# Performance work log

Hardware: AMD Instinct MI355X
Metric: run time of the kernel (lower is better)

Reference implementation:

```python
import jax, jax.numpy as jnp
import numpy as np
import math

B, R, Q, K, C = 1, 128, 256, 256, 256
H, D = 8, 32  # no_heads, c_hidden; H*D == C


def setup_inputs() -> dict:
    key = jax.random.key(0)
    ks = jax.random.split(key, 11)
    s = 0.02
    return {
        "q_x": jax.random.normal(ks[0], (B, R, Q, C), jnp.float32),
        "k_x": jax.random.normal(ks[1], (B, R, K, C), jnp.float32),
        "v_x": jax.random.normal(ks[2], (B, R, K, C), jnp.float32),
        "bias": jax.random.normal(ks[3], (1, 1, H, Q, K), jnp.float32),
        # weights stored [in, out] (equivalent to torch Linear weight.T)
        "Wq": jax.random.normal(ks[4], (C, H * D), jnp.float32) * s,
        "Wk": jax.random.normal(ks[5], (C, H * D), jnp.float32) * s,
        "Wv": jax.random.normal(ks[6], (C, H * D), jnp.float32) * s,
        "Wo": jax.random.normal(ks[7], (H * D, C), jnp.float32) * s,
        "bo": jax.random.normal(ks[8], (C,), jnp.float32) * s,
        "Wg": jax.random.normal(ks[9], (C, H * D), jnp.float32) * s,
        "bg": jnp.ones((H * D,), jnp.float32),  # gating init: bias = 1
    }


def reference(q_x, k_x, v_x, bias, Wq, Wk, Wv, Wo, bo, Wg, bg):
    norm = 1.0 / math.sqrt(D)
    # projections -> [*, S, H, D]
    q = (q_x @ Wq).reshape(*q_x.shape[:-1], H, D)
    k = (k_x @ Wk).reshape(*k_x.shape[:-1], H, D)
    v = (v_x @ Wv).reshape(*v_x.shape[:-1], H, D)
    # scaled logits [*, H, Q, K] plus external bias
    a = jnp.einsum("...qhd,...khd->...hqk", q, k) * norm + bias
    a = jax.nn.softmax(a, axis=-1)
    # [*, Q, H, D]
    o = jnp.einsum("...hqk,...khd->...qhd", a, v)
    # sigmoid gate from query data
    g = jax.nn.sigmoid(q_x @ Wg + bg).reshape(o.shape)
    o = o * g
    o = o.reshape(*o.shape[:-2], H * D)
    return o @ Wo + bo
```

## Files before the change

### kernel.cpp

```cpp
#include <hip/hip_runtime.h>
#include <hip/hip_bf16.h>
#include <cstdint>
#include <cstddef>

typedef __attribute__((ext_vector_type(8))) short short8;
typedef __attribute__((ext_vector_type(4))) short s16x4;
typedef __attribute__((ext_vector_type(4))) unsigned short u16x4;
typedef __attribute__((ext_vector_type(8))) unsigned short u16x8;
typedef __attribute__((ext_vector_type(4))) float f32x4;
typedef __attribute__((ext_vector_type(4))) unsigned int u32x4;

__device__ __forceinline__ short bfbits(float f) {
    __bf16 h = (__bf16)f;
    return __builtin_bit_cast(short, h);
}
__device__ __forceinline__ float bf2f(unsigned short b) {
    union { uint32_t u; float f; } v; v.u = ((uint32_t)b) << 16;
    return v.f;
}
__device__ __forceinline__ unsigned int pack2(float x, float y) {
    return (unsigned int)(unsigned short)bfbits(x) |
           ((unsigned int)(unsigned short)bfbits(y) << 16);
}

__global__ __launch_bounds__(256) void prep_kernel(
    const float* __restrict__ Wq, const float* __restrict__ Wk,
    const float* __restrict__ Wv, const float* __restrict__ Wg,
    const float* __restrict__ Wo, unsigned short* __restrict__ wt,
    const float* __restrict__ bias, float* __restrict__ bt)
{
    int bid = blockIdx.x;
    int tid = threadIdx.x;
    if (bid < 80) {
        int mat  = bid >> 4;
        int tile = bid & 15;
        int k0 = (tile >> 2) * 64, n0 = (tile & 3) * 64;
        const float* W = (mat==0)?Wq:(mat==1)?Wk:(mat==2)?Wv:(mat==3)?Wg:Wo;
        __shared__ unsigned short T[64][72];
        int tx = tid & 15, ty = tid >> 4;
        #pragma unroll
        for (int j = 0; j < 4; ++j) {
            int kr = ty + j*16;
            f32x4 v = *(const f32x4*)(W + (size_t)(k0+kr)*256 + n0 + tx*4);
            #pragma unroll
            for (int e = 0; e < 4; ++e) T[tx*4+e][kr] = (unsigned short)bfbits(v[e]);
        }
        __syncthreads();
        #pragma unroll
        for (int j = 0; j < 4; ++j) {
            int nr = ty + j*16;
            int kk = k0 + tx*4;
            int dstk = kk;
            if (mat == 4) {
                int a = (kk >> 2) & 7;
                int hb = kk & ~31;
                dstk = hb + ((a < 4) ? 8*a : 8*(a-4) + 4);
            }
            u16x4 st;
            #pragma unroll
            for (int e = 0; e < 4; ++e) st[e] = T[nr][tx*4+e];
            *(u16x4*)(wt + ((size_t)mat*256 + n0+nr)*256 + dstk) = st;
        }
    } else {
        int hb = bid - 80;
        int h = hb >> 4, qt = hb & 15;
        int cc = tid >> 4, n = tid & 15;
        const float* src = bias + ((size_t)(h*256 + qt*16 + cc))*256 + n*16;
        float* dst = bt + ((size_t)(hb*16 + n))*256 + cc*16;
        #pragma unroll
        for (int q = 0; q < 4; ++q)
            *(f32x4*)(dst + q*4) = *(const f32x4*)(src + q*4);
    }
}

template<int SWAP>
__device__ __forceinline__ void proj_mfma_loop2(
    const unsigned short* As, const unsigned short* Wt,
    int col0, int c, int g, f32x4 acc[4][2])
{
    short8 pb[2];
    #pragma unroll
    for (int n = 0; n < 2; ++n)
        pb[n] = *(const short8*)(Wt + (size_t)(col0 + n*16 + c) * 256 + g*8);

    #pragma unroll
    for (int step = 0; step < 8; ++step) {
        short8 b[2];
        #pragma unroll
        for (int n = 0; n < 2; ++n) b[n] = pb[n];
        if (step < 7) {
            int koff = (step + 1) * 32 + g * 8;
            #pragma unroll
            for (int n = 0; n < 2; ++n)
                pb[n] = *(const short8*)(Wt + (size_t)(col0 + n*16 + c) * 256 + koff);
        }
        short8 a[4];
        #pragma unroll
        for (int m = 0; m < 4; ++m) {
            int row = m * 16 + c;
            int off = row * 512 + ((step * 64 + g * 16) ^ ((row & 31) << 4));
            a[m] = *(const short8*)((const char*)As + off);
        }
        #pragma unroll
        for (int m = 0; m < 4; ++m)
            #pragma unroll
            for (int n = 0; n < 2; ++n) {
                if (SWAP)
                    acc[m][n] = __builtin_amdgcn_mfma_f32_16x16x32_bf16(b[n], a[m], acc[m][n], 0, 0, 0);
                else
                    acc[m][n] = __builtin_amdgcn_mfma_f32_16x16x32_bf16(a[m], b[n], acc[m][n], 0, 0, 0);
            }
    }
}

__global__ __launch_bounds__(512, 2) void proj_kernel(
    const float* __restrict__ qx, const float* __restrict__ kx, const float* __restrict__ vx,
    const float* __restrict__ bg, const unsigned short* __restrict__ wt,
    unsigned short* __restrict__ Qa, unsigned short* __restrict__ Ka,
    unsigned short* __restrict__ Va, unsigned short* __restrict__ G)
{
    __shared__ __align__(16) unsigned short As[2][64 * 256];

    int rb = blockIdx.x;
    int row0 = rb * 64;
    int tid = threadIdx.x;
    int w = tid >> 6, lane = tid & 63;
    int c = lane & 15, g = lane >> 4;
    int col0 = w * 32;
    int l32 = tid & 31, rg = tid >> 5;
    int r_ = row0 >> 8;
    int s0b = row0 & 255;
    int h_ = col0 >> 5;

    u32x4 pk[4], pn[4];

    #pragma unroll
    for (int j = 0; j < 4; ++j) {
        const float* src = qx + (size_t)(row0 + j*16 + rg) * 256 + l32 * 8;
        f32x4 lo = *(const f32x4*)src;
        f32x4 hi = *(const f32x4*)(src + 4);
        pk[j][0] = pack2(lo[0], lo[1]); pk[j][1] = pack2(lo[2], lo[3]);
        pk[j][2] = pack2(hi[0], hi[1]); pk[j][3] = pack2(hi[2], hi[3]);
    }

    #pragma unroll
    for (int j = 0; j < 4; ++j) {
        int row = j*16 + rg;
        int off = row * 512 + ((l32 * 16) ^ ((row & 31) << 4));
        *(u32x4*)((char*)&As[0][0] + off) = pk[j];
    }
    #pragma unroll
    for (int j = 0; j < 4; ++j) {
        const float* src = kx + (size_t)(row0 + j*16 + rg) * 256 + l32 * 8;
        f32x4 lo = *(const f32x4*)src;
        f32x4 hi = *(const f32x4*)(src + 4);
        pn[j][0] = pack2(lo[0], lo[1]); pn[j][1] = pack2(lo[2], lo[3]);
        pn[j][2] = pack2(hi[0], hi[1]); pn[j][3] = pack2(hi[2], hi[3]);
    }
    __syncthreads();
    {
        f32x4 acc[4][2];
        #pragma unroll
        for (int m = 0; m < 4; ++m)
            #pragma unroll
            for (int n = 0; n < 2; ++n) acc[m][n] = 0.0f;
        proj_mfma_loop2<1>(&As[0][0], wt, col0, c, g, acc);
        #pragma unroll
        for (int m = 0; m < 4; ++m) {
            int s_ = s0b + m * 16 + c;
            u16x8 st;
            #pragma unroll
            for (int i = 0; i < 4; ++i) {
                st[i]     = (unsigned short)bfbits(acc[m][0][i]);
                st[i + 4] = (unsigned short)bfbits(acc[m][1][i]);
            }
            *(u16x8*)(Qa + ((size_t)((r_*8 + h_)*256 + s_)) * 32 + 8*g) = st;
        }
        #pragma unroll
        for (int m = 0; m < 4; ++m)
            #pragma unroll
            for (int n = 0; n < 2; ++n) acc[m][n] = 0.0f;
        proj_mfma_loop2<1>(&As[0][0], wt + 3*65536, col0, c, g, acc);
        f32x4 bg0 = *(const f32x4*)(bg + col0 + 4*g);
        f32x4 bg1 = *(const f32x4*)(bg + col0 + 16 + 4*g);
        #pragma unroll
        for (int m = 0; m < 4; ++m) {
            int rq = row0 + m * 16 + c;
            u16x8 st;
            #pragma unroll
            for (int i = 0; i < 4; ++i) {
                float sa = 1.0f / (1.0f + __expf(-(acc[m][0][i] + bg0[i])));
                float sb = 1.0f / (1.0f + __expf(-(acc[m][1][i] + bg1[i])));
                st[i]     = (unsigned short)bfbits(sa);
                st[i + 4] = (unsigned short)bfbits(sb);
            }
            *(u16x8*)(G + (size_t)rq * 256 + col0 + 8*g) = st;
        }
    }

    #pragma unroll
    for (int j = 0; j < 4; ++j) {
        int row = j*16 + rg;
        int off = row * 512 + ((l32 * 16) ^ ((row & 31) << 4));
        *(u32x4*)((char*)&As[1][0] + off) = pn[j];
    }
    #pragma unroll
    for (int j = 0; j < 4; ++j) {
        const float* src = vx + (size_t)(row0 + j*16 + rg) * 256 + l32 * 8;
        f32x4 lo = *(const f32x4*)src;
        f32x4 hi = *(const f32x4*)(src + 4);
        pk[j][0] = pack2(lo[0], lo[1]); pk[j][1] = pack2(lo[2], lo[3]);
        pk[j][2] = pack2(hi[0], hi[1]); pk[j][3] = pack2(hi[2], hi[3]);
    }
    __syncthreads();
    {
        f32x4 acc[4][2];
        #pragma unroll
        for (int m = 0; m < 4; ++m)
            #pragma unroll
            for (int n = 0; n < 2; ++n) acc[m][n] = 0.0f;
        proj_mfma_loop2<1>(&As[1][0], wt + 65536, col0, c, g, acc);
        #pragma unroll
        for (int m = 0; m < 4; ++m) {
            int s_ = s0b + m * 16 + c;
            u16x8 st;
            #pragma unroll
            for (int i = 0; i < 4; ++i) {
                st[i]     = (unsigned short)bfbits(acc[m][0][i]);
                st[i + 4] = (unsigned short)bfbits(acc[m][1][i]);
            }
            *(u16x8*)(Ka + ((size_t)((r_*8 + h_)*256 + s_)) * 32 + 8*g) = st;
        }
    }

    #pragma unroll
    for (int j = 0; j < 4; ++j) {
        int row = j*16 + rg;
        int off = row * 512 + ((l32 * 16) ^ ((row & 31) << 4));
        *(u32x4*)((char*)&As[0][0] + off) = pk[j];
    }
    __syncthreads();
    {
        f32x4 acc[4][2];
        #pragma unroll
        for (int m = 0; m < 4; ++m)
            #pragma unroll
            for (int n = 0; n < 2; ++n) acc[m][n] = 0.0f;
        proj_mfma_loop2<0>(&As[0][0], wt + 2*65536, col0, c, g, acc);
        #pragma unroll
        for (int n = 0; n < 2; ++n) {
            int d_ = n*16 + c;
            size_t rowbase = ((size_t)((r_*8 + h_)*32 + d_)) * 256;
            #pragma unroll
            for (int p = 0; p < 2; ++p) {
                u16x8 st;
                #pragma unroll
                for (int i = 0; i < 4; ++i) {
                    st[i]     = (unsigned short)bfbits(acc[2*p][n][i]);
                    st[i + 4] = (unsigned short)bfbits(acc[2*p+1][n][i]);
                }
                *(u16x8*)(Va + rowbase + s0b + 32*p + 8*g) = st;
            }
        }
    }
}

__global__ __launch_bounds__(512) void attn_kernel(
    const unsigned short* __restrict__ Qa, const unsigned short* __restrict__ Ka,
    const unsigned short* __restrict__ Va, const unsigned short* __restrict__ G,
    const float* __restrict__ bt, unsigned short* __restrict__ og)
{
    __shared__ __align__(16) unsigned short Ks[256 * 40];
    __shared__ __align__(16) unsigned short Vs[32 * 264];

    int rh = blockIdx.x;
    int r = rh >> 3, h = rh & 7;
    int tid = threadIdx.x;
    int w = tid >> 6, lane = tid & 63;
    int c = lane & 15, g = lane >> 4;
    size_t base = (size_t)rh * 8192;

    #pragma unroll
    for (int j = 0; j < 2; ++j) {
        int idx8 = (tid + j*512) * 8;
        int s_ = idx8 >> 5, d_ = idx8 & 31;
        short8 v = *(const short8*)(Ka + base + idx8);
        *(short8*)(&Ks[s_*40 + d_]) = v;
    }
    #pragma unroll
    for (int j = 0; j < 2; ++j) {
        int idx8 = (tid + j*512) * 8;
        int d_ = idx8 >> 8, s0 = idx8 & 255;
        short8 v = *(const short8*)(Va + base + idx8);
        *(short8*)(&Vs[d_*264 + s0]) = v;
    }
    __syncthreads();

    const float* bth = bt + (size_t)h * 65536;
    const float nrmv = 0.17677669529663687f;

    #pragma unroll 1
    for (int qq = 0; qq < 2; ++qq) {
        int qt = w*2 + qq;
        int qrow = qt * 16;
        short8 qf = *(const short8*)(Qa + base + (size_t)(qrow + c)*32 + g*8);
        const float* btt = bth + (size_t)qt*4096 + (c*4 + g)*4;

        f32x4 o0 = 0.0f, o1 = 0.0f;
        float sum = 0.f;
        #pragma unroll
        for (int t = 0; t < 8; ++t) {
            int n0 = 2*t, n1 = 2*t + 1;
            short8 kf0 = *(const short8*)(&Ks[(n0*16 + c)*40 + g*8]);
            short8 kf1 = *(const short8*)(&Ks[(n1*16 + c)*40 + g*8]);
            f32x4 bv0 = *(const f32x4*)(btt + n0*256);
            f32x4 bv1 = *(const f32x4*)(btt + n1*256);
            f32x4 z = 0.0f;
            f32x4 s0 = __builtin_amdgcn_mfma_f32_16x16x32_bf16(kf0, qf, z, 0, 0, 0);
            f32x4 s1 = __builtin_amdgcn_mfma_f32_16x16x32_bf16(kf1, qf, z, 0, 0, 0);
            float e0 = __expf(fmaf(s0[0], nrmv, bv0[0]));
            float e1 = __expf(fmaf(s0[1], nrmv, bv0[1]));
            float e2 = __expf(fmaf(s0[2], nrmv, bv0[2]));
            float e3 = __expf(fmaf(s0[3], nrmv, bv0[3]));
            float e4 = __expf(fmaf(s1[0], nrmv, bv1[0]));
            float e5 = __expf(fmaf(s1[1], nrmv, bv1[1]));
            float e6 = __expf(fmaf(s1[2], nrmv, bv1[2]));
            float e7 = __expf(fmaf(s1[3], nrmv, bv1[3]));
            sum += ((e0+e1)+(e2+e3)) + ((e4+e5)+(e6+e7));
            u32x4 aw;
            aw[0] = pack2(e0, e1); aw[1] = pack2(e2, e3);
            aw[2] = pack2(e4, e5); aw[3] = pack2(e6, e7);
            short8 pfrag = __builtin_bit_cast(short8, aw);
            short8 va0 = *(const short8*)(&Vs[(c)*264      + t*32 + g*8]);
            short8 va1 = *(const short8*)(&Vs[(16 + c)*264 + t*32 + g*8]);
            o0 = __builtin_amdgcn_mfma_f32_16x16x32_bf16(va0, pfrag, o0, 0, 0, 0);
            o1 = __builtin_amdgcn_mfma_f32_16x16x32_bf16(va1, pfrag, o1, 0, 0, 0);
        }
        sum += __shfl_xor(sum, 16);
        sum += __shfl_xor(sum, 32);
        float inv = 1.0f / sum;

        size_t orow = ((size_t)(r*256 + qrow + c)) * 256 + h*32 + 8*g;
        u16x8 gv = *(const u16x8*)(G + orow);
        u16x8 st;
        #pragma unroll
        for (int i = 0; i < 4; ++i) {
            st[i]     = (unsigned short)bfbits(o0[i] * inv * bf2f(gv[i]));
            st[i + 4] = (unsigned short)bfbits(o1[i] * inv * bf2f(gv[i + 4]));
        }
        *(u16x8*)(og + orow) = st;
    }
}

__device__ __forceinline__ void proj_mfma_loop_swap(
    const unsigned short* As, const unsigned short* Wt,
    int col0, int c, int g, f32x4 acc[4][4])
{
    short8 pb[4];
    #pragma unroll
    for (int n = 0; n < 4; ++n)
        pb[n] = *(const short8*)(Wt + (size_t)(col0 + n*16 + c) * 256 + g*8);

    #pragma unroll
    for (int step = 0; step < 8; ++step) {
        short8 b[4];
        #pragma unroll
        for (int n = 0; n < 4; ++n) b[n] = pb[n];
        if (step < 7) {
            int koff = (step + 1) * 32 + g * 8;
            #pragma unroll
            for (int n = 0; n < 4; ++n)
                pb[n] = *(const short8*)(Wt + (size_t)(col0 + n*16 + c) * 256 + koff);
        }
        short8 a[4];
        #pragma unroll
        for (int m = 0; m < 4; ++m) {
            int row = m * 16 + c;
            int off = row * 512 + ((step * 64 + g * 16) ^ ((row & 31) << 4));
            a[m] = *(const short8*)((const char*)As + off);
        }
        #pragma unroll
        for (int m = 0; m < 4; ++m)
            #pragma unroll
            for (int n = 0; n < 4; ++n)
                acc[m][n] = __builtin_amdgcn_mfma_f32_16x16x32_bf16(b[n], a[m], acc[m][n], 0, 0, 0);
    }
}

__global__ __launch_bounds__(256) void oproj_kernel(
    const unsigned short* __restrict__ og, const unsigned short* __restrict__ wt_o,
    const float* __restrict__ bo, float* __restrict__ out)
{
    __shared__ __align__(16) unsigned short As[64 * 256];

    int row0 = blockIdx.x * 64;
    int tid = threadIdx.x;
    int lane = tid & 63;
    int c = lane & 15, g = lane >> 4;
    int col0 = (tid >> 6) * 64;

    #pragma unroll
    for (int j = 0; j < 8; ++j) {
        int idx = tid * 8 + j * 2048;
        int row = idx >> 8;
        int colB = (idx & 255) * 2;
        short8 v = *(const short8*)(og + (size_t)(row0 + row) * 256 + (idx & 255));
        int off = row * 512 + (colB ^ ((row & 31) << 4));
        *(short8*)((char*)As + off) = v;
    }
    __syncthreads();

    f32x4 acc[4][4];
    #pragma unroll
    for (int m = 0; m < 4; ++m)
        #pragma unroll
        for (int n = 0; n < 4; ++n)
            acc[m][n] = 0.0f;

    proj_mfma_loop_swap(As, wt_o, col0, c, g, acc);

    #pragma unroll
    for (int n = 0; n < 4; ++n) {
        int colb = col0 + n * 16 + 4 * g;
        f32x4 bov = *(const f32x4*)(bo + colb);
        #pragma unroll
        for (int m = 0; m < 4; ++m) {
            int row = row0 + m * 16 + c;
            f32x4 st = acc[m][n] + bov;
            *(f32x4*)(out + (size_t)row * 256 + colb) = st;
        }
    }
}

extern "C" void kernel_launch(void* const* d_in, const int* in_sizes, int n_in,
                              void* d_out, int out_size, void* d_ws, size_t ws_size,
                              hipStream_t stream) {
    const float* qx   = (const float*)d_in[0];
    const float* kx   = (const float*)d_in[1];
    const float* vx   = (const float*)d_in[2];
    const float* bias = (const float*)d_in[3];
    const float* Wq   = (const float*)d_in[4];
    const float* Wk   = (const float*)d_in[5];
    const float* Wv   = (const float*)d_in[6];
    const float* Wo   = (const float*)d_in[7];
    const float* bo   = (const float*)d_in[8];
    const float* Wg   = (const float*)d_in[9];
    const float* bg   = (const float*)d_in[10];

    uint8_t* ws = (uint8_t*)d_ws;
    unsigned short* wt = (unsigned short*)ws;
    unsigned short* Qa = (unsigned short*)(ws + (1u<<20));
    unsigned short* Ka = (unsigned short*)(ws + (1u<<20) + 1u*(1u<<24));
    unsigned short* Va = (unsigned short*)(ws + (1u<<20) + 2u*(1u<<24));
    unsigned short* G  = (unsigned short*)(ws + (1u<<20) + 3u*(1u<<24));
    unsigned short* og = (unsigned short*)(ws + (1u<<20) + 4u*(1u<<24));
    float*          bt = (float*)        (ws + (1u<<20) + 5u*(1u<<24));

    hipLaunchKernelGGL(prep_kernel, dim3(208), dim3(256), 0, stream,
                       Wq, Wk, Wv, Wg, Wo, wt, bias, bt);
    hipLaunchKernelGGL(proj_kernel, dim3(512), dim3(512), 0, stream,
                       qx, kx, vx, bg, wt, Qa, Ka, Va, G);
    hipLaunchKernelGGL(attn_kernel, dim3(1024), dim3(512), 0, stream,
                       Qa, Ka, Va, G, bt, og);
    hipLaunchKernelGGL(oproj_kernel, dim3(512), dim3(256), 0, stream,
                       og, wt + 4*65536, bo, (float*)d_out);
}
```

Baseline: 120.4 us.

## Fuse attention with output projection, accumulating per-head contributions in registers

Merges the attention and output-projection kernels: each block handles one row and 64 query rows, loops over all heads, and multiplies each head's gated attention output by the matching slice of Wo straight into register accumulators. This removes the bf16 intermediate round trip through global memory and one kernel launch. In exchange, each head's K/V tile is loaded four times (once per query block), the grid has fewer threads in total, and Wo fragments are fetched from global memory on every head iteration.

```diff
diff --git a/kernel.cpp b/kernel.cpp
--- a/kernel.cpp
+++ b/kernel.cpp
@@ -265,46 +265,49 @@
     }
 }
 
-__global__ __launch_bounds__(512) void attn_kernel(
+__global__ __launch_bounds__(256, 3) void attn_oproj_kernel(
     const unsigned short* __restrict__ Qa, const unsigned short* __restrict__ Ka,
     const unsigned short* __restrict__ Va, const unsigned short* __restrict__ G,
-    const float* __restrict__ bt, unsigned short* __restrict__ og)
+    const float* __restrict__ bt, const unsigned short* __restrict__ wt_o,
+    const float* __restrict__ bo, float* __restrict__ out)
 {
     __shared__ __align__(16) unsigned short Ks[256 * 40];
     __shared__ __align__(16) unsigned short Vs[32 * 264];
 
-    int rh = blockIdx.x;
-    int r = rh >> 3, h = rh & 7;
+    int bx = blockIdx.x;
+    int r = bx >> 2, qb = bx & 3;
     int tid = threadIdx.x;
     int w = tid >> 6, lane = tid & 63;
     int c = lane & 15, g = lane >> 4;
-    size_t base = (size_t)rh * 8192;
-
-    #pragma unroll
-    for (int j = 0; j < 2; ++j) {
-        int idx8 = (tid + j*512) * 8;
-        int s_ = idx8 >> 5, d_ = idx8 & 31;
-        short8 v = *(const short8*)(Ka + base + idx8);
-        *(short8*)(&Ks[s_*40 + d_]) = v;
-    }
-    #pragma unroll
-    for (int j = 0; j < 2; ++j) {
-        int idx8 = (tid + j*512) * 8;
-        int d_ = idx8 >> 8, s0 = idx8 & 255;
-        short8 v = *(const short8*)(Va + base + idx8);
-        *(short8*)(&Vs[d_*264 + s0]) = v;
-    }
-    __syncthreads();
-
-    const float* bth = bt + (size_t)h * 65536;
+    int qrow = qb * 64 + w * 16;
+    int qt = qb * 4 + w;
     const float nrmv = 0.17677669529663687f;
 
+    f32x4 acc[16];
+    #pragma unroll
+    for (int n = 0; n < 16; ++n)
+        acc[n] = *(const f32x4*)(bo + n*16 + 4*g);
+
     #pragma unroll 1
-    for (int qq = 0; qq < 2; ++qq) {
-        int qt = w*2 + qq;
-        int qrow = qt * 16;
+    for (int h = 0; h < 8; ++h) {
+        size_t base = ((size_t)(r*8 + h)) * 8192;
+
+        #pragma unroll
+        for (int j = 0; j < 4; ++j) {
+            int idx8 = (tid + j*256) * 8;
+            int s_ = idx8 >> 5, d_ = idx8 & 31;
+            *(short8*)(&Ks[s_*40 + d_]) = *(const short8*)(Ka + base + idx8);
+        }
+        #pragma unroll
+        for (int j = 0; j < 4; ++j) {
+            int idx8 = (tid + j*256) * 8;
+            int d_ = idx8 >> 8, s0 = idx8 & 255;
+            *(short8*)(&Vs[d_*264 + s0]) = *(const short8*)(Va + base + idx8);
+        }
+        __syncthreads();
+
         short8 qf = *(const short8*)(Qa + base + (size_t)(qrow + c)*32 + g*8);
-        const float* btt = bth + (size_t)qt*4096 + (c*4 + g)*4;
+        const float* btt = bt + (size_t)h*65536 + (size_t)qt*4096 + (c*4 + g)*4;
 
         f32x4 o0 = 0.0f, o1 = 0.0f;
         float sum = 0.f;
@@ -342,94 +345,27 @@
 
         size_t orow = ((size_t)(r*256 + qrow + c)) * 256 + h*32 + 8*g;
         u16x8 gv = *(const u16x8*)(G + orow);
-        u16x8 st;
+        u16x8 av;
         #pragma unroll
         for (int i = 0; i < 4; ++i) {
-            st[i]     = (unsigned short)bfbits(o0[i] * inv * bf2f(gv[i]));
-            st[i + 4] = (unsigned short)bfbits(o1[i] * inv * bf2f(gv[i + 4]));
-        }
-        *(u16x8*)(og + orow) = st;
-    }
-}
-
-__device__ __forceinline__ void proj_mfma_loop_swap(
-    const unsigned short* As, const unsigned short* Wt,
-    int col0, int c, int g, f32x4 acc[4][4])
-{
-    short8 pb[4];
-    #pragma unroll
-    for (int n = 0; n < 4; ++n)
-        pb[n] = *(const short8*)(Wt + (size_t)(col0 + n*16 + c) * 256 + g*8);
-
-    #pragma unroll
-    for (int step = 0; step < 8; ++step) {
-        short8 b[4];
-        #pragma unroll
-        for (int n = 0; n < 4; ++n) b[n] = pb[n];
-        if (step < 7) {
-            int koff = (step + 1) * 32 + g * 8;
-            #pragma unroll
-            for (int n = 0; n < 4; ++n)
-                pb[n] = *(const short8*)(Wt + (size_t)(col0 + n*16 + c) * 256 + koff);
-        }
-        short8 a[4];
-        #pragma unroll
-        for (int m = 0; m < 4; ++m) {
-            int row = m * 16 + c;
-            int off = row * 512 + ((step * 64 + g * 16) ^ ((row & 31) << 4));
-            a[m] = *(const short8*)((const char*)As + off);
-        }
-        #pragma unroll
-        for (int m = 0; m < 4; ++m)
-            #pragma unroll
-            for (int n = 0; n < 4; ++n)
-                acc[m][n] = __builtin_amdgcn_mfma_f32_16x16x32_bf16(b[n], a[m], acc[m][n], 0, 0, 0);
-    }
-}
-
-__global__ __launch_bounds__(256) void oproj_kernel(
-    const unsigned short* __restrict__ og, const unsigned short* __restrict__ wt_o,
-    const float* __restrict__ bo, float* __restrict__ out)
-{
-    __shared__ __align__(16) unsigned short As[64 * 256];
-
-    int row0 = blockIdx.x * 64;
-    int tid = threadIdx.x;
-    int lane = tid & 63;
-    int c = lane & 15, g = lane >> 4;
-    int col0 = (tid >> 6) * 64;
-
-    #pragma unroll
-    for (int j = 0; j < 8; ++j) {
-        int idx = tid * 8 + j * 2048;
-        int row = idx >> 8;
-        int colB = (idx & 255) * 2;
-        short8 v = *(const short8*)(og + (size_t)(row0 + row) * 256 + (idx & 255));
-        int off = row * 512 + (colB ^ ((row & 31) << 4));
-        *(short8*)((char*)As + off) = v;
-    }
-    __syncthreads();
-
-    f32x4 acc[4][4];
-    #pragma unroll
-    for (int m = 0; m < 4; ++m)
-        #pragma unroll
-        for (int n = 0; n < 4; ++n)
-            acc[m][n] = 0.0f;
-
-    proj_mfma_loop_swap(As, wt_o, col0, c, g, acc);
-
-    #pragma unroll
-    for (int n = 0; n < 4; ++n) {
-        int colb = col0 + n * 16 + 4 * g;
-        f32x4 bov = *(const f32x4*)(bo + colb);
-        #pragma unroll
-        for (int m = 0; m < 4; ++m) {
-            int row = row0 + m * 16 + c;
-            f32x4 st = acc[m][n] + bov;
-            *(f32x4*)(out + (size_t)row * 256 + colb) = st;
-        }
-    }
+            av[i]     = (unsigned short)bfbits(o0[i] * inv * bf2f(gv[i]));
+            av[i + 4] = (unsigned short)bfbits(o1[i] * inv * bf2f(gv[i + 4]));
+        }
+        short8 afrag = __builtin_bit_cast(short8, av);
+
+        const unsigned short* wo = wt_o + 32*h + g*8;
+        #pragma unroll
+        for (int n = 0; n < 16; ++n) {
+            short8 b = *(const short8*)(wo + (size_t)(n*16 + c) * 256);
+            acc[n] = __builtin_amdgcn_mfma_f32_16x16x32_bf16(b, afrag, acc[n], 0, 0, 0);
+        }
+        __syncthreads();
+    }
+
+    float* orow_out = out + (size_t)(r*256 + qrow + c) * 256 + 4*g;
+    #pragma unroll
+    for (int n = 0; n < 16; ++n)
+        *(f32x4*)(orow_out + n*16) = acc[n];
 }
 
 extern "C" void kernel_launch(void* const* d_in, const int* in_sizes, int n_in,
@@ -453,15 +389,12 @@
     unsigned short* Ka = (unsigned short*)(ws + (1u<<20) + 1u*(1u<<24));
     unsigned short* Va = (unsigned short*)(ws + (1u<<20) + 2u*(1u<<24));
     unsigned short* G  = (unsigned short*)(ws + (1u<<20) + 3u*(1u<<24));
-    unsigned short* og = (unsigned short*)(ws + (1u<<20) + 4u*(1u<<24));
     float*          bt = (float*)        (ws + (1u<<20) + 5u*(1u<<24));
 
     hipLaunchKernelGGL(prep_kernel, dim3(208), dim3(256), 0, stream,
                        Wq, Wk, Wv, Wg, Wo, wt, bias, bt);
     hipLaunchKernelGGL(proj_kernel, dim3(512), dim3(512), 0, stream,
                        qx, kx, vx, bg, wt, Qa, Ka, Va, G);
-    hipLaunchKernelGGL(attn_kernel, dim3(1024), dim3(512), 0, stream,
-                       Qa, Ka, Va, G, bt, og);
-    hipLaunchKernelGGL(oproj_kernel, dim3(512), dim3(256), 0, stream,
-                       og, wt + 4*65536, bo, (float*)d_out);
-}
+    hipLaunchKernelGGL(attn_oproj_kernel, dim3(512), dim3(256), 0, stream,
+                       Qa, Ka, Va, G, bt, wt + 4*65536, bo, (float*)d_out);
+}
```

After: 146.7 us. 1.22x slower.
